# Kernel tuning notes

Hardware: AMD Instinct MI355X
Metric: run time of the kernel (lower is better)

Reference implementation:

```python
import jax, jax.numpy as jnp
import numpy as np

EPS = 1e-5
SLOPE = 0.01  # LeakyReLU default negative_slope
D_STATE = 16


def leaky(x):
    return jnp.where(x >= 0, x, SLOPE * x)


def instance_norm(x):
    # InstanceNorm3d(affine=False): normalize per (n, c) over spatial dims
    m = x.mean(axis=(2, 3, 4), keepdims=True)
    v = x.var(axis=(2, 3, 4), keepdims=True)
    return (x - m) * jax.lax.rsqrt(v + EPS)


def conv3d(x, w, b, groups=1, pad=0):
    y = jax.lax.conv_general_dilated(
        x, w, (1, 1, 1), [(pad, pad)] * 3,
        dimension_numbers=('NCDHW', 'OIDHW', 'NCDHW'),
        feature_group_count=groups)
    return y + b[None, :, None, None, None]


def conv_transpose2(x, w, b):
    # ConvTranspose3d(k=2, s=2): non-overlapping, so it is a pure einsum+interleave
    # x: [n,c,d,h,w], w: [c,o,2,2,2] (torch layout)
    y = jnp.einsum('ncdhw,coijk->nodihjwk', x, w)
    n, o, d, _, h, _, ww, _ = y.shape
    return y.reshape(n, o, 2 * d, 2 * h, 2 * ww) + b[None, :, None, None, None]


def selective_scan(u, dt, A, B, C, D):
    # u, dt: [b,l,d]; A: [d,n]; B, C: [b,l,n]; D: [d]
    dA = jnp.exp(dt[..., None] * A)                              # [b,l,d,n]
    dBu = dt[..., None] * B[:, :, None, :] * u[..., None]        # [b,l,d,n]

    def step(h, inp):
        dA_t, dBu_t, C_t = inp
        h = dA_t * h + dBu_t                                     # [b,d,n]
        y = jnp.einsum('bdn,bn->bd', h, C_t)
        return h, y

    h0 = jnp.zeros((u.shape[0],) + A.shape, u.dtype)
    _, ys = jax.lax.scan(
        step, h0,
        (dA.transpose(1, 0, 2, 3), dBu.transpose(1, 0, 2, 3), C.transpose(1, 0, 2)))
    return ys.transpose(1, 0, 2) + u * D                         # [b,l,d]


def mamba_block(x, in_proj_w, conv1d_w, conv1d_b, x_proj_w,
                dt_proj_w, dt_proj_b, A_log, D_param, out_proj_w):
    # x: [b,l,c]
    dt_rank = dt_proj_w.shape[1]
    xz = x @ in_proj_w.T                                         # [b,l,2*d_inner]
    xi, z = jnp.split(xz, 2, axis=-1)
    # causal depthwise conv1d over sequence (torch pads d_conv-1 both sides, keeps [:L])
    xi_c = xi.transpose(0, 2, 1)                                 # [b,d_inner,l]
    xi_c = jax.lax.conv_general_dilated(
        xi_c, conv1d_w, (1,), [(conv1d_w.shape[-1] - 1, 0)],
        dimension_numbers=('NCH', 'OIH', 'NCH'),
        feature_group_count=xi_c.shape[1])
    xi = jax.nn.silu(xi_c + conv1d_b[None, :, None]).transpose(0, 2, 1)  # [b,l,d_inner]
    x_dbl = xi @ x_proj_w.T
    dt, B, C = jnp.split(x_dbl, [dt_rank, dt_rank + D_STATE], axis=-1)
    dt = jax.nn.softplus(dt @ dt_proj_w.T + dt_proj_b)
    A = -jnp.exp(A_log)
    y = selective_scan(xi, dt, A, B, C, D_param)
    y = y * jax.nn.silu(z)
    return y @ out_proj_w.T


def layer_norm(x, w, b):
    m = x.mean(-1, keepdims=True)
    v = x.var(-1, keepdims=True)
    return (x - m) * jax.lax.rsqrt(v + EPS) * w + b


def up_forward(x1, x2, up_w, up_b, dc1_w, dc1_b, dc2_w, dc2_b, dc3_w, dc3_b,
               ln_w, ln_b, in_proj_w, conv1d_w, conv1d_b, x_proj_w,
               dt_proj_w, dt_proj_b, A_log, D_param, out_proj_w):
    x1 = conv_transpose2(x1, up_w, up_b)
    dZ = x2.shape[2] - x1.shape[2]
    dY = x2.shape[3] - x1.shape[3]
    dX = x2.shape[4] - x1.shape[4]
    x1 = jnp.pad(x1, ((0, 0), (0, 0),
                      (dZ // 2, dZ - dZ // 2),
                      (dY // 2, dY - dY // 2),
                      (dX // 2, dX - dX // 2)))
    x = jnp.concatenate([x2, x1], axis=1)
    # DoubleConv (residual=False since in_channels != out_channels)
    x = leaky(instance_norm(conv3d(x, dc1_w, dc1_b)))
    x = leaky(instance_norm(conv3d(x, dc2_w, dc2_b, groups=8, pad=1)))
    x = leaky(instance_norm(conv3d(x, dc3_w, dc3_b)))
    # MambaLayer over flattened spatial tokens
    b, c, d, h, w = x.shape
    t = x.transpose(0, 2, 3, 4, 1).reshape(b, d * h * w, c)
    t = layer_norm(t, ln_w, ln_b)
    t = mamba_block(t, in_proj_w, conv1d_w, conv1d_b, x_proj_w,
                    dt_proj_w, dt_proj_b, A_log, D_param, out_proj_w)
    return t.reshape(b, d, h, w, c).transpose(0, 4, 1, 2, 3)


def setup_inputs() -> dict:
    key = jax.random.key(0)
    ks = jax.random.split(key, 20)
    c_out = 32      # out_channels / d_model
    d_inner = 64    # expand * d_model
    dt_rank = 2     # ceil(32/16)
    s = 0.02
    return {
        'x1': jax.random.normal(ks[0], (2, 32, 8, 16, 16), jnp.float32),
        'x2': jax.random.normal(ks[1], (2, 32, 16, 32, 32), jnp.float32),
        'up_w': jax.random.normal(ks[2], (32, 32, 2, 2, 2), jnp.float32) * s,
        'up_b': jnp.zeros((32,), jnp.float32),
        'dc1_w': jax.random.normal(ks[3], (32, 64, 1, 1, 1), jnp.float32) * s,
        'dc1_b': jnp.zeros((32,), jnp.float32),
        'dc2_w': jax.random.normal(ks[4], (32, 4, 3, 3, 3), jnp.float32) * s,
        'dc2_b': jnp.zeros((32,), jnp.float32),
        'dc3_w': jax.random.normal(ks[5], (32, 32, 1, 1, 1), jnp.float32) * s,
        'dc3_b': jnp.zeros((32,), jnp.float32),
        'ln_w': jnp.ones((c_out,), jnp.float32),
        'ln_b': jnp.zeros((c_out,), jnp.float32),
        'in_proj_w': jax.random.normal(ks[6], (2 * d_inner, c_out), jnp.float32) * s,
        'conv1d_w': jax.random.normal(ks[7], (d_inner, 1, 4), jnp.float32) * s,
        'conv1d_b': jnp.zeros((d_inner,), jnp.float32),
        'x_proj_w': jax.random.normal(ks[8], (dt_rank + 2 * D_STATE, d_inner), jnp.float32) * s,
        'dt_proj_w': jax.random.normal(ks[9], (d_inner, dt_rank), jnp.float32) * s,
        'dt_proj_b': jnp.full((d_inner,), -4.0, jnp.float32),
        'A_log': jnp.log(jnp.tile(jnp.arange(1.0, D_STATE + 1.0, dtype=jnp.float32), (d_inner, 1))),
        'D_param': jnp.ones((d_inner,), jnp.float32),
        'out_proj_w': jax.random.normal(ks[10], (c_out, d_inner), jnp.float32) * s,
    }


def reference(x1, x2, up_w, up_b, dc1_w, dc1_b, dc2_w, dc2_b, dc3_w, dc3_b,
              ln_w, ln_b, in_proj_w, conv1d_w, conv1d_b, x_proj_w,
              dt_proj_w, dt_proj_b, A_log, D_param, out_proj_w):
    return up_forward(x1, x2, up_w, up_b, dc1_w, dc1_b, dc2_w, dc2_b, dc3_w, dc3_b,
                      ln_w, ln_b, in_proj_w, conv1d_w, conv1d_b, x_proj_w,
                      dt_proj_w, dt_proj_b, A_log, D_param, out_proj_w)
```

## Files before the change

### kernel.cpp

```cpp
#include <hip/hip_runtime.h>

#define TPB 256
#define BATCH 2
#define S_TOT 16384
#define NST 16
#define NCHUNK 256
#define CLEN 64
#define EPS 1e-5f
#define SLOPE 0.01f

__device__ __forceinline__ float leakyf(float v){ return v > 0.f ? v : SLOPE * v; }
__device__ __forceinline__ float siluf(float v){ return v / (1.f + __expf(-v)); }

__global__ __launch_bounds__(TPB) void k_up(
    const float* __restrict__ x1, const float* __restrict__ upw,
    const float* __restrict__ upb, float* __restrict__ up) {
  __shared__ float wq[2048];
  int t = threadIdx.x;
  int idx = blockIdx.x * TPB + t;
  int s = idx & 16383;
  int n = (idx >> 14) & 1;
  int q = idx >> 15;
  for (int i = t; i < 2048; i += TPB) {
    int c = i >> 6;
    wq[i] = upw[c*256 + q*64 + (i & 63)];
  }
  __syncthreads();
  int z = s >> 10, y = (s >> 5) & 31, x = s & 31;
  int tap = ((z & 1)*2 + (y & 1))*2 + (x & 1);
  int xb = n*65536 + (z >> 1)*256 + (y >> 1)*16 + (x >> 1);
  float xv[32];
  #pragma unroll
  for (int c = 0; c < 32; c++) xv[c] = x1[xb + c*2048];
  float acc[8];
  #pragma unroll
  for (int j = 0; j < 8; j++) acc[j] = upb[q*8 + j];
  #pragma unroll
  for (int c = 0; c < 32; c++) {
    #pragma unroll
    for (int j = 0; j < 8; j++)
      acc[j] += xv[c] * wq[c*64 + j*8 + tap];
  }
  #pragma unroll
  for (int j = 0; j < 8; j++)
    up[(n*32 + q*8 + j)*S_TOT + s] = acc[j];
}

__global__ __launch_bounds__(TPB) void k_conv1(
    const float* __restrict__ x2, const float* __restrict__ up,
    const float* __restrict__ w, const float* __restrict__ bias,
    float* __restrict__ c1, float* __restrict__ st1) {
  __shared__ float ws[512];
  __shared__ float red[4][8][2];
  int t = threadIdx.x;
  int idx = blockIdx.x * TPB + t;
  int s = idx & 16383;
  int n = (idx >> 14) & 1;
  int q = idx >> 15;
  int c0 = q*8;
  for (int i = t; i < 512; i += TPB) ws[i] = w[c0*64 + i];
  __syncthreads();
  const float* px2 = x2 + n*32*S_TOT + s;
  const float* pup = up + n*32*S_TOT + s;
  float acc[8];
  #pragma unroll
  for (int j = 0; j < 8; j++) acc[j] = bias[c0 + j];
  #pragma unroll
  for (int i = 0; i < 32; i++) {
    float v = px2[i*S_TOT];
    #pragma unroll
    for (int j = 0; j < 8; j++) acc[j] += v * ws[j*64 + i];
  }
  #pragma unroll
  for (int i = 0; i < 32; i++) {
    float v = pup[i*S_TOT];
    #pragma unroll
    for (int j = 0; j < 8; j++) acc[j] += v * ws[j*64 + 32 + i];
  }
  #pragma unroll
  for (int j = 0; j < 8; j++)
    c1[(n*32 + c0 + j)*S_TOT + s] = acc[j];
  int wv = t >> 6;
  #pragma unroll
  for (int j = 0; j < 8; j++) {
    float sm = acc[j], sq = acc[j]*acc[j];
    #pragma unroll
    for (int o = 32; o > 0; o >>= 1) { sm += __shfl_down(sm, o); sq += __shfl_down(sq, o); }
    if ((t & 63) == 0) { red[wv][j][0] = sm; red[wv][j][1] = sq; }
  }
  __syncthreads();
  if (t < 16) {
    int j = t >> 1, m = t & 1;
    float a = red[0][j][m] + red[1][j][m] + red[2][j][m] + red[3][j][m];
    atomicAdd(&st1[(n*32 + c0 + j)*2 + m], a);
  }
}

__global__ __launch_bounds__(TPB) void k_pad(
    const float* __restrict__ c1, const float* __restrict__ st1,
    float* __restrict__ pn) {
  int slice = blockIdx.y;
  int i = blockIdx.x * TPB + threadIdx.x;
  if (i >= 20808) return;
  float s0 = st1[slice*2], s1 = st1[slice*2 + 1];
  float m = s0 * (1.f/S_TOT);
  float rs = rsqrtf(s1*(1.f/S_TOT) - m*m + EPS);
  int zp = i / 1156; int r = i - zp*1156; int yp = r / 34; int xp = r - yp*34;
  float v = 0.f;
  if (zp >= 1 && zp <= 16 && yp >= 1 && yp <= 32 && xp >= 1 && xp <= 32)
    v = leakyf((c1[slice*S_TOT + (zp-1)*1024 + (yp-1)*32 + (xp-1)] - m) * rs);
  pn[slice*20808 + i] = v;
}

__global__ __launch_bounds__(TPB) void k_conv2(
    const float* __restrict__ pn, const float* __restrict__ w,
    const float* __restrict__ bias, float* __restrict__ c2,
    float* __restrict__ st2) {
  __shared__ float ws[432];
  __shared__ float red[4][4][2];
  int bid = blockIdx.x, t = threadIdx.x;
  int s = ((bid & 63) << 8) + t;
  int g = (bid >> 6) & 7;
  int n = bid >> 9;
  for (int i = t; i < 432; i += TPB) ws[i] = w[(g*4)*108 + i];
  __syncthreads();
  int z = s >> 10, y = (s >> 5) & 31, x = s & 31;
  float acc[4];
  #pragma unroll
  for (int oc = 0; oc < 4; oc++) acc[oc] = bias[g*4 + oc];
  const float* pbase = pn + ((n*32 + g*4)*18)*1156;
  #pragma unroll
  for (int ic = 0; ic < 4; ic++) {
    const float* pc = pbase + ic*(18*1156);
    #pragma unroll
    for (int dz = 0; dz < 3; dz++) {
      #pragma unroll
      for (int dy = 0; dy < 3; dy++) {
        const float* pr = pc + (z+dz)*1156 + (y+dy)*34 + x;
        float p0 = pr[0], p1 = pr[1], p2 = pr[2];
        int wb = ic*27 + dz*9 + dy*3;
        #pragma unroll
        for (int oc = 0; oc < 4; oc++) {
          const float* wo = &ws[oc*108 + wb];
          acc[oc] += p0*wo[0] + p1*wo[1] + p2*wo[2];
        }
      }
    }
  }
  float sm[4], sq[4];
  #pragma unroll
  for (int oc = 0; oc < 4; oc++) {
    c2[(n*32 + g*4 + oc)*S_TOT + s] = acc[oc];
    sm[oc] = acc[oc]; sq[oc] = acc[oc]*acc[oc];
  }
  #pragma unroll
  for (int o = 32; o > 0; o >>= 1) {
    #pragma unroll
    for (int oc = 0; oc < 4; oc++) {
      sm[oc] += __shfl_down(sm[oc], o);
      sq[oc] += __shfl_down(sq[oc], o);
    }
  }
  int lane = t & 63, wv = t >> 6;
  if (lane == 0) {
    #pragma unroll
    for (int oc = 0; oc < 4; oc++) { red[wv][oc][0] = sm[oc]; red[wv][oc][1] = sq[oc]; }
  }
  __syncthreads();
  if (t < 8) {
    int oc = t & 3, m = t >> 2;
    float a = red[0][oc][m] + red[1][oc][m] + red[2][oc][m] + red[3][oc][m];
    atomicAdd(&st2[(n*32 + g*4 + oc)*2 + m], a);
  }
}

__global__ __launch_bounds__(TPB) void k_conv3(
    const float* __restrict__ c2, const float* __restrict__ w,
    const float* __restrict__ bias, const float* __restrict__ st2,
    float* __restrict__ c3, float* __restrict__ st3) {
  __shared__ float ws[256];
  __shared__ float mrs[32][2];
  __shared__ float red[4][8][2];
  int t = threadIdx.x;
  int idx = blockIdx.x * TPB + t;
  int s = idx & 16383;
  int n = (idx >> 14) & 1;
  int q = idx >> 15;
  int c0 = q*8;
  if (t < 256) ws[t] = w[c0*32 + t];
  if (t < 32) {
    float s0 = st2[(n*32+t)*2], s1 = st2[(n*32+t)*2+1];
    float m = s0 * (1.f/S_TOT);
    mrs[t][0] = m; mrs[t][1] = rsqrtf(s1*(1.f/S_TOT) - m*m + EPS);
  }
  __syncthreads();
  const float* pin = c2 + n*32*S_TOT + s;
  float acc[8];
  #pragma unroll
  for (int j = 0; j < 8; j++) acc[j] = bias[c0 + j];
  #pragma unroll
  for (int i = 0; i < 32; i++) {
    float v = leakyf((pin[i*S_TOT] - mrs[i][0]) * mrs[i][1]);
    #pragma unroll
    for (int j = 0; j < 8; j++) acc[j] += v * ws[j*32 + i];
  }
  #pragma unroll
  for (int j = 0; j < 8; j++)
    c3[(n*32 + c0 + j)*S_TOT + s] = acc[j];
  int wv = t >> 6;
  #pragma unroll
  for (int j = 0; j < 8; j++) {
    float sm = acc[j], sq = acc[j]*acc[j];
    #pragma unroll
    for (int o = 32; o > 0; o >>= 1) { sm += __shfl_down(sm, o); sq += __shfl_down(sq, o); }
    if ((t & 63) == 0) { red[wv][j][0] = sm; red[wv][j][1] = sq; }
  }
  __syncthreads();
  if (t < 16) {
    int j = t >> 1, m = t & 1;
    float a = red[0][j][m] + red[1][j][m] + red[2][j][m] + red[3][j][m];
    atomicAdd(&st3[(n*32 + c0 + j)*2 + m], a);
  }
}

__global__ __launch_bounds__(TPB) void k_inproj(
    const float* __restrict__ c3, const float* __restrict__ st3,
    const float* __restrict__ lnw, const float* __restrict__ lnb,
    const float* __restrict__ ipw,
    float* __restrict__ xi, float* __restrict__ zb) {
  __shared__ float W2T[4096];
  __shared__ float tk[16*33];
  __shared__ float S1[128], S2[128];
  __shared__ float mv[16][2];
  __shared__ float mrs[32][2];
  int t = threadIdx.x;
  int token0 = blockIdx.x * 16;
  int n = token0 >> 14;
  int s0 = token0 & 16383;
  if (t < 32) {
    float a = st3[(n*32+t)*2], b = st3[(n*32+t)*2+1];
    float m = a * (1.f/S_TOT);
    mrs[t][0] = m; mrs[t][1] = rsqrtf(b*(1.f/S_TOT) - m*m + EPS);
  }
  __syncthreads();
  for (int i = t; i < 4096; i += TPB) {
    int f = i >> 5, c = i & 31;
    W2T[c*128 + f] = ipw[i] * lnw[c];
  }
  for (int i = t; i < 512; i += TPB) {
    int c = i >> 4, lt = i & 15;
    float raw = c3[(n*32 + c)*S_TOT + s0 + lt];
    tk[lt*33 + c] = leakyf((raw - mrs[c][0]) * mrs[c][1]);
  }
  __syncthreads();
  if (t < 128) {
    float a = 0.f, b = 0.f;
    #pragma unroll
    for (int c = 0; c < 32; c++) { a += W2T[c*128 + t]; b += ipw[t*32 + c]*lnb[c]; }
    S1[t] = a; S2[t] = b;
  }
  if (t < 16) {
    float mean = 0.f;
    #pragma unroll
    for (int c = 0; c < 32; c++) mean += tk[t*33 + c];
    mean *= (1.f/32.f);
    float var = 0.f;
    #pragma unroll
    for (int c = 0; c < 32; c++) { float d = tk[t*33 + c] - mean; var += d*d; }
    mv[t][0] = mean; mv[t][1] = rsqrtf(var*(1.f/32.f) + EPS);
  }
  __syncthreads();
  int f = t & 127, half = t >> 7;
  for (int lt = half; lt < 16; lt += 2) {
    float acc = 0.f;
    #pragma unroll
    for (int c = 0; c < 32; c++) acc += W2T[c*128 + f] * tk[lt*33 + c];
    float r = mv[lt][1]*(acc - mv[lt][0]*S1[f]) + S2[f];
    int token = token0 + lt;
    if (f < 64) xi[token*64 + f] = r;
    else        zb[token*64 + (f - 64)] = r;
  }
}

__global__ __launch_bounds__(TPB) void k_conv1d(
    const float* __restrict__ xi, const float* __restrict__ c1w,
    const float* __restrict__ c1b, const float* __restrict__ xpw,
    const float* __restrict__ dtw, const float* __restrict__ dtbi,
    float* __restrict__ u, float* __restrict__ dt,
    float* __restrict__ Bb, float* __restrict__ Cc) {
  __shared__ float xpT[2176];
  __shared__ float uu[16*64];
  __shared__ float xd[16*34];
  int t = threadIdx.x;
  int token0 = blockIdx.x * 16;
  for (int i = t; i < 2176; i += TPB) { int f = i >> 6, dd = i & 63; xpT[dd*34 + f] = xpw[i]; }
  int ch = t & 63;
  float cw0 = c1w[ch*4], cw1 = c1w[ch*4+1], cw2 = c1w[ch*4+2], cw3 = c1w[ch*4+3];
  float cb = c1b[ch];
  #pragma unroll
  for (int r = 0; r < 4; r++) {
    int lt = (t >> 6) + 4*r;
    int token = token0 + lt;
    int n = token >> 14, s = token & 16383;
    int base = (n << 14)*64;
    float acc = cb;
    float v0 = (s >= 3) ? xi[base + (s-3)*64 + ch] : 0.f;
    float v1 = (s >= 2) ? xi[base + (s-2)*64 + ch] : 0.f;
    float v2 = (s >= 1) ? xi[base + (s-1)*64 + ch] : 0.f;
    float v3 = xi[base + s*64 + ch];
    acc += v0*cw0 + v1*cw1 + v2*cw2 + v3*cw3;
    float uv = siluf(acc);
    u[token*64 + ch] = uv;
    uu[lt*64 + ch] = uv;
  }
  __syncthreads();
  for (int i = t; i < 544; i += TPB) {
    int lt = i / 34; int f = i - lt*34;
    float a = 0.f;
    #pragma unroll
    for (int dd = 0; dd < 64; dd++) a += xpT[dd*34 + f] * uu[lt*64 + dd];
    xd[lt*34 + f] = a;
  }
  __syncthreads();
  float dw0 = dtw[ch*2], dw1 = dtw[ch*2+1], dbv = dtbi[ch];
  #pragma unroll
  for (int r = 0; r < 4; r++) {
    int lt = (t >> 6) + 4*r;
    int token = token0 + lt;
    float dv = xd[lt*34]*dw0 + xd[lt*34+1]*dw1 + dbv;
    dt[token*64 + ch] = fmaxf(dv, 0.f) + log1pf(__expf(-fabsf(dv)));
    if (ch < 16)      Bb[token*16 + ch]      = xd[lt*34 + 2 + ch];
    else if (ch < 32) Cc[token*16 + ch - 16] = xd[lt*34 + 2 + ch];
  }
}


__global__ __launch_bounds__(TPB) void k_scan1(
    const float* __restrict__ dt, const float* __restrict__ u,
    const float* __restrict__ Bb, const float* __restrict__ Alog,
    float* __restrict__ cA, float* __restrict__ cX) {
  __shared__ __align__(16) float sdt[1024], su[1024], sB[256];
  int bid = blockIdx.x, t = threadIdx.x;
  int chunk = bid & 255, b = bid >> 8;
  int q = t & 3, d = t >> 2;
  float Ar[4];
  #pragma unroll
  for (int j = 0; j < 4; j++) Ar[j] = -__expf(Alog[d*16 + 4*q + j]);
  float h[4] = {0.f,0.f,0.f,0.f};
  float sdts = 0.f;
  int tg0 = b*S_TOT + chunk*CLEN;
  for (int tile = 0; tile < 4; tile++) {
    int base = tg0 + tile*16;
    for (int i = t; i < 1024; i += TPB) { sdt[i] = dt[base*64 + i]; su[i] = u[base*64 + i]; }
    sB[t] = Bb[base*16 + t];
    __syncthreads();
    #pragma unroll
    for (int tt = 0; tt < 16; tt++) {
      float dtv = sdt[tt*64 + d], uv = su[tt*64 + d];
      sdts += dtv;
      float du = dtv * uv;
      float4 Bq = *(const float4*)(sB + tt*16 + q*4);
      h[0] = __expf(Ar[0]*dtv)*h[0] + Bq.x*du;
      h[1] = __expf(Ar[1]*dtv)*h[1] + Bq.y*du;
      h[2] = __expf(Ar[2]*dtv)*h[2] + Bq.z*du;
      h[3] = __expf(Ar[3]*dtv)*h[3] + Bq.w*du;
    }
    __syncthreads();
  }
  #pragma unroll
  for (int j = 0; j < 4; j++) {
    int idx = (((b*64 + d)*16 + 4*q + j)*NCHUNK) + chunk;
    cA[idx] = __expf(Ar[j]*sdts);
    cX[idx] = h[j];
  }
}

__global__ __launch_bounds__(TPB) void k_scan2(
    const float* __restrict__ cA, float* __restrict__ cX) {
  int t = threadIdx.x;
  int w = blockIdx.x*4 + (t >> 6);
  int lane = t & 63;
  int b = w >> 10, d = (w >> 4) & 63, nn = w & 15;
  int base = ((b*64 + d)*16 + nn)*NCHUNK;
  float4 a = *(const float4*)(cA + base + lane*4);
  float4 x = *(const float4*)(cX + base + lane*4);
  float A = a.x*a.y*a.z*a.w;
  float X = ((x.x*a.y + x.y)*a.z + x.z)*a.w + x.w;
  #pragma unroll
  for (int off = 1; off < 64; off <<= 1) {
    float Ap = __shfl_up(A, off);
    float Xp = __shfl_up(X, off);
    if (lane >= off) { X = A*Xp + X; A = A*Ap; }
  }
  float Xe = __shfl_up(X, 1);
  if (lane == 0) Xe = 0.f;
  float r = Xe;
  float4 o;
  o.x = r; r = a.x*r + x.x;
  o.y = r; r = a.y*r + x.y;
  o.z = r; r = a.z*r + x.z;
  o.w = r;
  *(float4*)(cX + base + lane*4) = o;
}

__global__ __launch_bounds__(TPB) void k_scan3(
    const float* __restrict__ dt, const float* __restrict__ u,
    const float* __restrict__ Bb, const float* __restrict__ Cc,
    const float* __restrict__ Alog, const float* __restrict__ Dp,
    const float* __restrict__ zb, const float* __restrict__ cX,
    float* __restrict__ g) {
  __shared__ __align__(16) float sdt[1024], su[1024], sz[1024], sB[256], sC[256];
  int bid = blockIdx.x, t = threadIdx.x;
  int chunk = bid & 255, b = bid >> 8;
  int q = t & 3, d = t >> 2;
  float Ar[4];
  #pragma unroll
  for (int j = 0; j < 4; j++) Ar[j] = -__expf(Alog[d*16 + 4*q + j]);
  float h[4];
  #pragma unroll
  for (int j = 0; j < 4; j++)
    h[j] = cX[(((b*64 + d)*16 + 4*q + j)*NCHUNK) + chunk];
  float Dv = Dp[d];
  int tg0 = b*S_TOT + chunk*CLEN;
  float* grow = g + (b*64 + d)*S_TOT + chunk*CLEN;
  for (int tile = 0; tile < 4; tile++) {
    int base = tg0 + tile*16;
    for (int i = t; i < 1024; i += TPB) {
      sdt[i] = dt[base*64 + i]; su[i] = u[base*64 + i]; sz[i] = zb[base*64 + i];
    }
    sB[t] = Bb[base*16 + t];
    sC[t] = Cc[base*16 + t];
    __syncthreads();
    #pragma unroll
    for (int tt = 0; tt < 16; tt++) {
      float dtv = sdt[tt*64 + d], uv = su[tt*64 + d];
      float du = dtv * uv;
      float4 Bq = *(const float4*)(sB + tt*16 + q*4);
      float4 Cq = *(const float4*)(sC + tt*16 + q*4);
      h[0] = __expf(Ar[0]*dtv)*h[0] + Bq.x*du;
      h[1] = __expf(Ar[1]*dtv)*h[1] + Bq.y*du;
      h[2] = __expf(Ar[2]*dtv)*h[2] + Bq.z*du;
      h[3] = __expf(Ar[3]*dtv)*h[3] + Bq.w*du;
      float yp = h[0]*Cq.x + h[1]*Cq.y + h[2]*Cq.z + h[3]*Cq.w;
      yp += __shfl_xor(yp, 1);
      yp += __shfl_xor(yp, 2);
      if (q == 0) {
        float zv = sz[tt*64 + d];
        grow[tile*16 + tt] = (yp + uv*Dv) * siluf(zv);
      }
    }
    __syncthreads();
  }
}

__global__ __launch_bounds__(TPB) void k_out(
    const float* __restrict__ g, const float* __restrict__ opw,
    float* __restrict__ out) {
  __shared__ float ws[512];
  int t = threadIdx.x;
  int idx = blockIdx.x * TPB + t;
  int s = idx & 16383;
  int n = (idx >> 14) & 1;
  int q = idx >> 15;
  int c0 = q*8;
  for (int i = t; i < 512; i += TPB) ws[i] = opw[c0*64 + i];
  __syncthreads();
  const float* pg = g + n*64*S_TOT + s;
  float acc[8] = {0.f,0.f,0.f,0.f,0.f,0.f,0.f,0.f};
  #pragma unroll
  for (int dd = 0; dd < 64; dd++) {
    float v = pg[dd*S_TOT];
    #pragma unroll
    for (int j = 0; j < 8; j++) acc[j] += v * ws[j*64 + dd];
  }
  #pragma unroll
  for (int j = 0; j < 8; j++)
    out[(n*32 + c0 + j)*S_TOT + s] = acc[j];
}

extern "C" void kernel_launch(void* const* d_in, const int* in_sizes, int n_in,
                              void* d_out, int out_size, void* d_ws, size_t ws_size,
                              hipStream_t stream) {
  const float* x1    = (const float*)d_in[0];
  const float* x2    = (const float*)d_in[1];
  const float* upw   = (const float*)d_in[2];
  const float* upb   = (const float*)d_in[3];
  const float* dc1w  = (const float*)d_in[4];
  const float* dc1b  = (const float*)d_in[5];
  const float* dc2w  = (const float*)d_in[6];
  const float* dc2b  = (const float*)d_in[7];
  const float* dc3w  = (const float*)d_in[8];
  const float* dc3b  = (const float*)d_in[9];
  const float* lnw   = (const float*)d_in[10];
  const float* lnb   = (const float*)d_in[11];
  const float* ipw   = (const float*)d_in[12];
  const float* c1w   = (const float*)d_in[13];
  const float* c1b   = (const float*)d_in[14];
  const float* xpw   = (const float*)d_in[15];
  const float* dtw   = (const float*)d_in[16];
  const float* dtbi  = (const float*)d_in[17];
  const float* Alog  = (const float*)d_in[18];
  const float* Dp    = (const float*)d_in[19];
  const float* opw   = (const float*)d_in[20];
  float* out = (float*)d_out;

  float* ws = (float*)d_ws;
  float* ubuf = ws + 0;
  float* c1   = ws + 1048576;
  float* pn   = ws + 2097152;
  float* c2   = ws + 3428864;
  float* c3   = ws + 0;
  float* xi   = ws + 1048576;
  float* zb   = ws + 4477440;
  float* ub   = ws + 6574592;
  float* dtb  = ws + 8671744;
  float* Bb   = ws + 3428864;
  float* Cc   = ws + 3953152;
  float* cA   = ws + 0;
  float* cX   = ws + 524288;
  float* gbuf = ws + 1048576;
  float* st   = ws + 10768896;
  float* st1 = st, *st2 = st + 128, *st3 = st + 256;

  hipMemsetAsync(st, 0, 384*sizeof(float), stream);
  k_up     <<<512,  TPB, 0, stream>>>(x1, upw, upb, ubuf);
  k_conv1  <<<512,  TPB, 0, stream>>>(x2, ubuf, dc1w, dc1b, c1, st1);
  k_pad    <<<dim3(82,64), TPB, 0, stream>>>(c1, st1, pn);
  k_conv2  <<<1024, TPB, 0, stream>>>(pn, dc2w, dc2b, c2, st2);
  k_conv3  <<<512,  TPB, 0, stream>>>(c2, dc3w, dc3b, st2, c3, st3);
  k_inproj <<<2048, TPB, 0, stream>>>(c3, st3, lnw, lnb, ipw, xi, zb);
  k_conv1d <<<2048, TPB, 0, stream>>>(xi, c1w, c1b, xpw, dtw, dtbi, ub, dtb, Bb, Cc);
  k_scan1  <<<512,  TPB, 0, stream>>>(dtb, ub, Bb, Alog, cA, cX);
  k_scan2  <<<512,  TPB, 0, stream>>>(cA, cX);
  k_scan3  <<<512,  TPB, 0, stream>>>(dtb, ub, Bb, Cc, Alog, Dp, zb, cX, gbuf);
  k_out    <<<512,  TPB, 0, stream>>>(gbuf, opw, out);
}
```

Baseline: 247.0 us.

## Fuse pipeline into five kernels with grid-synced single-pass scan

Fuses the transposed-conv upsample into conv1, removes the padded-normalize pass by applying InstanceNorm and zero padding inside conv2, and merges in_proj with conv1d/x_proj/dt using a 3-token halo. The three scan kernels and the output projection become one persistent kernel that uses spin-wait barriers on global atomic counters for the cross-chunk carry scan. Instance-norm statistics move from atomics to per-block partial buffers reduced by the consumer kernel. This cuts launches and intermediate global traffic. The spin barriers depend on all 512 blocks being co-resident, and the counters are reset in the previous kernel.

New measurement: 372.5 us. 1.51x slower.

```diff
diff --git a/kernel.cpp b/kernel.cpp
--- a/kernel.cpp
+++ b/kernel.cpp
@@ -1,30 +1,27 @@
 #include <hip/hip_runtime.h>
 
 #define TPB 256
-#define BATCH 2
 #define S_TOT 16384
-#define NST 16
-#define NCHUNK 256
-#define CLEN 64
 #define EPS 1e-5f
 #define SLOPE 0.01f
 
 __device__ __forceinline__ float leakyf(float v){ return v > 0.f ? v : SLOPE * v; }
 __device__ __forceinline__ float siluf(float v){ return v / (1.f + __expf(-v)); }
 
-__global__ __launch_bounds__(TPB) void k_up(
-    const float* __restrict__ x1, const float* __restrict__ upw,
-    const float* __restrict__ upb, float* __restrict__ up) {
-  __shared__ float wq[2048];
-  int t = threadIdx.x;
-  int idx = blockIdx.x * TPB + t;
-  int s = idx & 16383;
-  int n = (idx >> 14) & 1;
-  int q = idx >> 15;
-  for (int i = t; i < 2048; i += TPB) {
-    int c = i >> 6;
-    wq[i] = upw[c*256 + q*64 + (i & 63)];
-  }
+__global__ __launch_bounds__(TPB) void k_upc1(
+    const float* __restrict__ x1, const float* __restrict__ x2,
+    const float* __restrict__ upw, const float* __restrict__ upb,
+    const float* __restrict__ w1, const float* __restrict__ b1,
+    float* __restrict__ c1, float* st1p) {
+  __shared__ float wq[8192];
+  __shared__ float ws[512];
+  __shared__ float sup[64*33];
+  __shared__ float red[4][8][2];
+  int t = threadIdx.x, bid = blockIdx.x;
+  int sb = bid & 255, n = bid >> 8;
+  int p = t & 63, os = t >> 6;
+  int s = sb*64 + p;
+  for (int i = t; i < 8192; i += TPB) wq[i] = upw[i];
   __syncthreads();
   int z = s >> 10, y = (s >> 5) & 31, x = s & 31;
   int tap = ((z & 1)*2 + (y & 1))*2 + (x & 1);
@@ -32,50 +29,35 @@
   float xv[32];
   #pragma unroll
   for (int c = 0; c < 32; c++) xv[c] = x1[xb + c*2048];
+  float up[8];
+  #pragma unroll
+  for (int j = 0; j < 8; j++) up[j] = upb[os*8 + j];
+  #pragma unroll
+  for (int c = 0; c < 32; c++) {
+    #pragma unroll
+    for (int j = 0; j < 8; j++)
+      up[j] += xv[c] * wq[c*256 + (os*8 + j)*8 + tap];
+  }
+  #pragma unroll
+  for (int j = 0; j < 8; j++) sup[p*33 + os*8 + j] = up[j];
+  for (int i = t; i < 512; i += TPB) ws[i] = 0.f;
+  __syncthreads();
+  int c0 = os*8;
   float acc[8];
   #pragma unroll
-  for (int j = 0; j < 8; j++) acc[j] = upb[q*8 + j];
-  #pragma unroll
-  for (int c = 0; c < 32; c++) {
-    #pragma unroll
-    for (int j = 0; j < 8; j++)
-      acc[j] += xv[c] * wq[c*64 + j*8 + tap];
-  }
-  #pragma unroll
-  for (int j = 0; j < 8; j++)
-    up[(n*32 + q*8 + j)*S_TOT + s] = acc[j];
-}
-
-__global__ __launch_bounds__(TPB) void k_conv1(
-    const float* __restrict__ x2, const float* __restrict__ up,
-    const float* __restrict__ w, const float* __restrict__ bias,
-    float* __restrict__ c1, float* __restrict__ st1) {
-  __shared__ float ws[512];
-  __shared__ float red[4][8][2];
-  int t = threadIdx.x;
-  int idx = blockIdx.x * TPB + t;
-  int s = idx & 16383;
-  int n = (idx >> 14) & 1;
-  int q = idx >> 15;
-  int c0 = q*8;
-  for (int i = t; i < 512; i += TPB) ws[i] = w[c0*64 + i];
-  __syncthreads();
+  for (int j = 0; j < 8; j++) acc[j] = b1[c0 + j];
   const float* px2 = x2 + n*32*S_TOT + s;
-  const float* pup = up + n*32*S_TOT + s;
-  float acc[8];
-  #pragma unroll
-  for (int j = 0; j < 8; j++) acc[j] = bias[c0 + j];
   #pragma unroll
   for (int i = 0; i < 32; i++) {
     float v = px2[i*S_TOT];
     #pragma unroll
-    for (int j = 0; j < 8; j++) acc[j] += v * ws[j*64 + i];
-  }
-  #pragma unroll
-  for (int i = 0; i < 32; i++) {
-    float v = pup[i*S_TOT];
-    #pragma unroll
-    for (int j = 0; j < 8; j++) acc[j] += v * ws[j*64 + 32 + i];
+    for (int j = 0; j < 8; j++) acc[j] += v * w1[(c0 + j)*64 + i];
+  }
+  #pragma unroll
+  for (int o = 0; o < 32; o++) {
+    float v = sup[p*33 + o];
+    #pragma unroll
+    for (int j = 0; j < 8; j++) acc[j] += v * w1[(c0 + j)*64 + 32 + o];
   }
   #pragma unroll
   for (int j = 0; j < 8; j++)
@@ -89,55 +71,67 @@
     if ((t & 63) == 0) { red[wv][j][0] = sm; red[wv][j][1] = sq; }
   }
   __syncthreads();
-  if (t < 16) {
-    int j = t >> 1, m = t & 1;
-    float a = red[0][j][m] + red[1][j][m] + red[2][j][m] + red[3][j][m];
-    atomicAdd(&st1[(n*32 + c0 + j)*2 + m], a);
+  if (t < 64) {
+    int w2 = t >> 4, j = (t >> 1) & 7, m = t & 1;
+    st1p[((n*32 + w2*8 + j)*2 + m)*256 + sb] = red[w2][j][m];
   }
 }
 
-__global__ __launch_bounds__(TPB) void k_pad(
-    const float* __restrict__ c1, const float* __restrict__ st1,
-    float* __restrict__ pn) {
-  int slice = blockIdx.y;
-  int i = blockIdx.x * TPB + threadIdx.x;
-  if (i >= 20808) return;
-  float s0 = st1[slice*2], s1 = st1[slice*2 + 1];
-  float m = s0 * (1.f/S_TOT);
-  float rs = rsqrtf(s1*(1.f/S_TOT) - m*m + EPS);
-  int zp = i / 1156; int r = i - zp*1156; int yp = r / 34; int xp = r - yp*34;
-  float v = 0.f;
-  if (zp >= 1 && zp <= 16 && yp >= 1 && yp <= 32 && xp >= 1 && xp <= 32)
-    v = leakyf((c1[slice*S_TOT + (zp-1)*1024 + (yp-1)*32 + (xp-1)] - m) * rs);
-  pn[slice*20808 + i] = v;
-}
-
 __global__ __launch_bounds__(TPB) void k_conv2(
-    const float* __restrict__ pn, const float* __restrict__ w,
-    const float* __restrict__ bias, float* __restrict__ c2,
-    float* __restrict__ st2) {
+    const float* __restrict__ c1, const float* __restrict__ w,
+    const float* __restrict__ bias, const float* st1p,
+    float* __restrict__ c2, float* st2p) {
   __shared__ float ws[432];
+  __shared__ float smom[4][2];
+  __shared__ float mrs[4][2];
   __shared__ float red[4][4][2];
   int bid = blockIdx.x, t = threadIdx.x;
-  int s = ((bid & 63) << 8) + t;
-  int g = (bid >> 6) & 7;
-  int n = bid >> 9;
+  int sb = bid & 63, g = (bid >> 6) & 7, n = bid >> 9;
+  int s = (sb << 8) + t;
   for (int i = t; i < 432; i += TPB) ws[i] = w[(g*4)*108 + i];
+  {
+    int pp = t >> 5, l = t & 31;
+    if (pp < 8) {
+      int j = pp & 3, m = pp >> 2;
+      const float* sp = st1p + ((n*32 + g*4 + j)*2 + m)*256;
+      float v = 0.f;
+      #pragma unroll
+      for (int k = 0; k < 8; k++) v += sp[l + 32*k];
+      v += __shfl_down(v, 16); v += __shfl_down(v, 8); v += __shfl_down(v, 4);
+      v += __shfl_down(v, 2);  v += __shfl_down(v, 1);
+      if (l == 0) smom[j][m] = v;
+    }
+  }
+  __syncthreads();
+  if (t < 4) {
+    float m = smom[t][0] * (1.f/S_TOT);
+    mrs[t][0] = m; mrs[t][1] = rsqrtf(smom[t][1]*(1.f/S_TOT) - m*m + EPS);
+  }
   __syncthreads();
   int z = s >> 10, y = (s >> 5) & 31, x = s & 31;
+  float mx0 = (x > 0) ? 1.f : 0.f, mx2 = (x < 31) ? 1.f : 0.f;
   float acc[4];
   #pragma unroll
   for (int oc = 0; oc < 4; oc++) acc[oc] = bias[g*4 + oc];
-  const float* pbase = pn + ((n*32 + g*4)*18)*1156;
+  const float* pbase = c1 + (n*32 + g*4)*S_TOT;
   #pragma unroll
   for (int ic = 0; ic < 4; ic++) {
-    const float* pc = pbase + ic*(18*1156);
+    const float* pc = pbase + ic*S_TOT;
+    float m = mrs[ic][0], rs = mrs[ic][1];
     #pragma unroll
     for (int dz = 0; dz < 3; dz++) {
+      int zz = z + dz - 1;
+      int zc = zz < 0 ? 0 : (zz > 15 ? 15 : zz);
+      float vz = (zz >= 0 && zz < 16) ? 1.f : 0.f;
       #pragma unroll
       for (int dy = 0; dy < 3; dy++) {
-        const float* pr = pc + (z+dz)*1156 + (y+dy)*34 + x;
-        float p0 = pr[0], p1 = pr[1], p2 = pr[2];
+        int yy = y + dy - 1;
+        int yc = yy < 0 ? 0 : (yy > 31 ? 31 : yy);
+        float vzy = vz * ((yy >= 0 && yy < 32) ? 1.f : 0.f);
+        const float* pr = pc + zc*1024 + yc*32 + x;
+        float p0 = leakyf((pr[-1] - m)*rs) * (vzy*mx0);
+        float p1 = leakyf((pr[ 0] - m)*rs) * vzy;
+        float p2 = leakyf((pr[ 1] - m)*rs) * (vzy*mx2);
         int wb = ic*27 + dz*9 + dy*3;
         #pragma unroll
         for (int oc = 0; oc < 4; oc++) {
@@ -170,15 +164,16 @@
   if (t < 8) {
     int oc = t & 3, m = t >> 2;
     float a = red[0][oc][m] + red[1][oc][m] + red[2][oc][m] + red[3][oc][m];
-    atomicAdd(&st2[(n*32 + g*4 + oc)*2 + m], a);
+    st2p[((n*32 + g*4 + oc)*2 + m)*64 + sb] = a;
   }
 }
 
 __global__ __launch_bounds__(TPB) void k_conv3(
     const float* __restrict__ c2, const float* __restrict__ w,
-    const float* __restrict__ bias, const float* __restrict__ st2,
-    float* __restrict__ c3, float* __restrict__ st3) {
+    const float* __restrict__ bias, const float* st2p,
+    float* __restrict__ c3, float* st3p) {
   __shared__ float ws[256];
+  __shared__ float ssum[32][2];
   __shared__ float mrs[32][2];
   __shared__ float red[4][8][2];
   int t = threadIdx.x;
@@ -186,12 +181,21 @@
   int s = idx & 16383;
   int n = (idx >> 14) & 1;
   int q = idx >> 15;
+  int sb = blockIdx.x & 63;
   int c0 = q*8;
   if (t < 256) ws[t] = w[c0*32 + t];
+  if (t < 64) {
+    int c = t >> 1, m = t & 1;
+    const float* sp = st2p + ((n*32 + c)*2 + m)*64;
+    float v = 0.f;
+    #pragma unroll
+    for (int k = 0; k < 64; k++) v += sp[k];
+    ssum[c][m] = v;
+  }
+  __syncthreads();
   if (t < 32) {
-    float s0 = st2[(n*32+t)*2], s1 = st2[(n*32+t)*2+1];
-    float m = s0 * (1.f/S_TOT);
-    mrs[t][0] = m; mrs[t][1] = rsqrtf(s1*(1.f/S_TOT) - m*m + EPS);
+    float m = ssum[t][0] * (1.f/S_TOT);
+    mrs[t][0] = m; mrs[t][1] = rsqrtf(ssum[t][1]*(1.f/S_TOT) - m*m + EPS);
   }
   __syncthreads();
   const float* pin = c2 + n*32*S_TOT + s;
@@ -219,263 +223,248 @@
   if (t < 16) {
     int j = t >> 1, m = t & 1;
     float a = red[0][j][m] + red[1][j][m] + red[2][j][m] + red[3][j][m];
-    atomicAdd(&st3[(n*32 + c0 + j)*2 + m], a);
+    st3p[((n*32 + c0 + j)*2 + m)*64 + sb] = a;
   }
 }
 
-__global__ __launch_bounds__(TPB) void k_inproj(
-    const float* __restrict__ c3, const float* __restrict__ st3,
+__global__ __launch_bounds__(TPB) void k_token(
+    const float* __restrict__ c3, const float* st3p,
     const float* __restrict__ lnw, const float* __restrict__ lnb,
-    const float* __restrict__ ipw,
-    float* __restrict__ xi, float* __restrict__ zb) {
+    const float* __restrict__ ipw, const float* __restrict__ c1w,
+    const float* __restrict__ c1b, const float* __restrict__ xpw,
+    const float* __restrict__ dtw, const float* __restrict__ dtbi,
+    float* __restrict__ zb, float* __restrict__ u, float* __restrict__ dt,
+    float* __restrict__ Bb, float* __restrict__ Cc, int* ctrs) {
   __shared__ float W2T[4096];
-  __shared__ float tk[16*33];
+  __shared__ float xpT[2176];
+  __shared__ float tk[19*33];
+  __shared__ float sxi[19*64];
+  __shared__ float su2[16*65];
+  __shared__ float xd[16*34];
   __shared__ float S1[128], S2[128];
-  __shared__ float mv[16][2];
+  __shared__ float mv[19][2];
   __shared__ float mrs[32][2];
-  int t = threadIdx.x;
-  int token0 = blockIdx.x * 16;
-  int n = token0 >> 14;
-  int s0 = token0 & 16383;
-  if (t < 32) {
-    float a = st3[(n*32+t)*2], b = st3[(n*32+t)*2+1];
-    float m = a * (1.f/S_TOT);
-    mrs[t][0] = m; mrs[t][1] = rsqrtf(b*(1.f/S_TOT) - m*m + EPS);
-  }
-  __syncthreads();
+  __shared__ float ssum[32][2];
+  int t = threadIdx.x, bid = blockIdx.x;
+  if (bid == 0 && t < 16) ctrs[t] = 0;
+  int tok0 = bid * 16;
+  int n = tok0 >> 14, s0 = tok0 & 16383;
+  if (t < 64) {
+    int c = t >> 1, m = t & 1;
+    const float* sp = st3p + ((n*32 + c)*2 + m)*64;
+    float v = 0.f;
+    #pragma unroll
+    for (int k = 0; k < 64; k++) v += sp[k];
+    ssum[c][m] = v;
+  }
   for (int i = t; i < 4096; i += TPB) {
     int f = i >> 5, c = i & 31;
     W2T[c*128 + f] = ipw[i] * lnw[c];
   }
-  for (int i = t; i < 512; i += TPB) {
-    int c = i >> 4, lt = i & 15;
-    float raw = c3[(n*32 + c)*S_TOT + s0 + lt];
+  for (int i = t; i < 2176; i += TPB) {
+    int f = i >> 6, dd = i & 63;
+    xpT[dd*34 + f] = xpw[i];
+  }
+  __syncthreads();
+  if (t < 32) {
+    float m = ssum[t][0] * (1.f/S_TOT);
+    mrs[t][0] = m; mrs[t][1] = rsqrtf(ssum[t][1]*(1.f/S_TOT) - m*m + EPS);
+  }
+  if (t < 128) {
+    float a = 0.f, b2 = 0.f;
+    #pragma unroll
+    for (int c = 0; c < 32; c++) { a += W2T[c*128 + t]; b2 += ipw[t*32 + c]*lnb[c]; }
+    S1[t] = a; S2[t] = b2;
+  }
+  __syncthreads();
+  for (int i = t; i < 608; i += TPB) {
+    int lt = i >> 5, c = i & 31;
+    int sg = s0 - 3 + lt;
+    int sgc = sg < 0 ? 0 : sg;
+    float raw = c3[(n*32 + c)*S_TOT + sgc];
     tk[lt*33 + c] = leakyf((raw - mrs[c][0]) * mrs[c][1]);
   }
   __syncthreads();
-  if (t < 128) {
-    float a = 0.f, b = 0.f;
-    #pragma unroll
-    for (int c = 0; c < 32; c++) { a += W2T[c*128 + t]; b += ipw[t*32 + c]*lnb[c]; }
-    S1[t] = a; S2[t] = b;
-  }
-  if (t < 16) {
+  if (t < 19) {
     float mean = 0.f;
     #pragma unroll
     for (int c = 0; c < 32; c++) mean += tk[t*33 + c];
     mean *= (1.f/32.f);
     float var = 0.f;
     #pragma unroll
-    for (int c = 0; c < 32; c++) { float d = tk[t*33 + c] - mean; var += d*d; }
+    for (int c = 0; c < 32; c++) { float d2 = tk[t*33 + c] - mean; var += d2*d2; }
     mv[t][0] = mean; mv[t][1] = rsqrtf(var*(1.f/32.f) + EPS);
   }
   __syncthreads();
-  int f = t & 127, half = t >> 7;
-  for (int lt = half; lt < 16; lt += 2) {
+  for (int i = t; i < 19*128; i += TPB) {
+    int lt = i >> 7, f = i & 127;
     float acc = 0.f;
     #pragma unroll
     for (int c = 0; c < 32; c++) acc += W2T[c*128 + f] * tk[lt*33 + c];
     float r = mv[lt][1]*(acc - mv[lt][0]*S1[f]) + S2[f];
-    int token = token0 + lt;
-    if (f < 64) xi[token*64 + f] = r;
-    else        zb[token*64 + (f - 64)] = r;
-  }
-}
-
-__global__ __launch_bounds__(TPB) void k_conv1d(
-    const float* __restrict__ xi, const float* __restrict__ c1w,
-    const float* __restrict__ c1b, const float* __restrict__ xpw,
-    const float* __restrict__ dtw, const float* __restrict__ dtbi,
-    float* __restrict__ u, float* __restrict__ dt,
-    float* __restrict__ Bb, float* __restrict__ Cc) {
-  __shared__ float xpT[2176];
-  __shared__ float uu[16*64];
-  __shared__ float xd[16*34];
-  int t = threadIdx.x;
-  int token0 = blockIdx.x * 16;
-  for (int i = t; i < 2176; i += TPB) { int f = i >> 6, dd = i & 63; xpT[dd*34 + f] = xpw[i]; }
+    int sg = s0 - 3 + lt;
+    if (f < 64) {
+      sxi[lt*64 + f] = (sg < 0) ? 0.f : r;
+    } else if (lt >= 3) {
+      zb[(tok0 + lt - 3)*64 + (f - 64)] = r;
+    }
+  }
+  __syncthreads();
   int ch = t & 63;
   float cw0 = c1w[ch*4], cw1 = c1w[ch*4+1], cw2 = c1w[ch*4+2], cw3 = c1w[ch*4+3];
   float cb = c1b[ch];
   #pragma unroll
   for (int r = 0; r < 4; r++) {
     int lt = (t >> 6) + 4*r;
-    int token = token0 + lt;
-    int n = token >> 14, s = token & 16383;
-    int base = (n << 14)*64;
-    float acc = cb;
-    float v0 = (s >= 3) ? xi[base + (s-3)*64 + ch] : 0.f;
-    float v1 = (s >= 2) ? xi[base + (s-2)*64 + ch] : 0.f;
-    float v2 = (s >= 1) ? xi[base + (s-1)*64 + ch] : 0.f;
-    float v3 = xi[base + s*64 + ch];
-    acc += v0*cw0 + v1*cw1 + v2*cw2 + v3*cw3;
+    float acc = cb + sxi[lt*64 + ch]*cw0 + sxi[(lt+1)*64 + ch]*cw1
+                   + sxi[(lt+2)*64 + ch]*cw2 + sxi[(lt+3)*64 + ch]*cw3;
     float uv = siluf(acc);
-    u[token*64 + ch] = uv;
-    uu[lt*64 + ch] = uv;
+    u[(tok0 + lt)*64 + ch] = uv;
+    su2[lt*65 + ch] = uv;
   }
   __syncthreads();
   for (int i = t; i < 544; i += TPB) {
-    int lt = i / 34; int f = i - lt*34;
+    int lt = i / 34, f = i - lt*34;
     float a = 0.f;
     #pragma unroll
-    for (int dd = 0; dd < 64; dd++) a += xpT[dd*34 + f] * uu[lt*64 + dd];
+    for (int dd = 0; dd < 64; dd++) a += xpT[dd*34 + f] * su2[lt*65 + dd];
     xd[lt*34 + f] = a;
   }
   __syncthreads();
-  float dw0 = dtw[ch*2], dw1 = dtw[ch*2+1], dbv = dtbi[ch];
+  float dw0 = dtw[ch*2], dw1 = dtw[ch*2+1], db = dtbi[ch];
   #pragma unroll
   for (int r = 0; r < 4; r++) {
     int lt = (t >> 6) + 4*r;
-    int token = token0 + lt;
-    float dv = xd[lt*34]*dw0 + xd[lt*34+1]*dw1 + dbv;
+    int token = tok0 + lt;
+    float dv = xd[lt*34]*dw0 + xd[lt*34 + 1]*dw1 + db;
     dt[token*64 + ch] = fmaxf(dv, 0.f) + log1pf(__expf(-fabsf(dv)));
     if (ch < 16)      Bb[token*16 + ch]      = xd[lt*34 + 2 + ch];
     else if (ch < 32) Cc[token*16 + ch - 16] = xd[lt*34 + 2 + ch];
   }
 }
 
-
-__global__ __launch_bounds__(TPB) void k_scan1(
-    const float* __restrict__ dt, const float* __restrict__ u,
-    const float* __restrict__ Bb, const float* __restrict__ Alog,
-    float* __restrict__ cA, float* __restrict__ cX) {
-  __shared__ __align__(16) float sdt[1024], su[1024], sB[256];
-  int bid = blockIdx.x, t = threadIdx.x;
-  int chunk = bid & 255, b = bid >> 8;
-  int q = t & 3, d = t >> 2;
-  float Ar[4];
-  #pragma unroll
-  for (int j = 0; j < 4; j++) Ar[j] = -__expf(Alog[d*16 + 4*q + j]);
-  float h[4] = {0.f,0.f,0.f,0.f};
-  float sdts = 0.f;
-  int tg0 = b*S_TOT + chunk*CLEN;
-  for (int tile = 0; tile < 4; tile++) {
-    int base = tg0 + tile*16;
-    for (int i = t; i < 1024; i += TPB) { sdt[i] = dt[base*64 + i]; su[i] = u[base*64 + i]; }
-    sB[t] = Bb[base*16 + t];
-    __syncthreads();
-    #pragma unroll
-    for (int tt = 0; tt < 16; tt++) {
-      float dtv = sdt[tt*64 + d], uv = su[tt*64 + d];
-      sdts += dtv;
-      float du = dtv * uv;
-      float4 Bq = *(const float4*)(sB + tt*16 + q*4);
-      h[0] = __expf(Ar[0]*dtv)*h[0] + Bq.x*du;
-      h[1] = __expf(Ar[1]*dtv)*h[1] + Bq.y*du;
-      h[2] = __expf(Ar[2]*dtv)*h[2] + Bq.z*du;
-      h[3] = __expf(Ar[3]*dtv)*h[3] + Bq.w*du;
-    }
-    __syncthreads();
-  }
-  #pragma unroll
-  for (int j = 0; j < 4; j++) {
-    int idx = (((b*64 + d)*16 + 4*q + j)*NCHUNK) + chunk;
-    cA[idx] = __expf(Ar[j]*sdts);
-    cX[idx] = h[j];
-  }
-}
-
-__global__ __launch_bounds__(TPB) void k_scan2(
-    const float* __restrict__ cA, float* __restrict__ cX) {
-  int t = threadIdx.x;
-  int w = blockIdx.x*4 + (t >> 6);
-  int lane = t & 63;
-  int b = w >> 10, d = (w >> 4) & 63, nn = w & 15;
-  int base = ((b*64 + d)*16 + nn)*NCHUNK;
-  float4 a = *(const float4*)(cA + base + lane*4);
-  float4 x = *(const float4*)(cX + base + lane*4);
-  float A = a.x*a.y*a.z*a.w;
-  float X = ((x.x*a.y + x.y)*a.z + x.z)*a.w + x.w;
-  #pragma unroll
-  for (int off = 1; off < 64; off <<= 1) {
-    float Ap = __shfl_up(A, off);
-    float Xp = __shfl_up(X, off);
-    if (lane >= off) { X = A*Xp + X; A = A*Ap; }
-  }
-  float Xe = __shfl_up(X, 1);
-  if (lane == 0) Xe = 0.f;
-  float r = Xe;
-  float4 o;
-  o.x = r; r = a.x*r + x.x;
-  o.y = r; r = a.y*r + x.y;
-  o.z = r; r = a.z*r + x.z;
-  o.w = r;
-  *(float4*)(cX + base + lane*4) = o;
-}
-
-__global__ __launch_bounds__(TPB) void k_scan3(
+__global__ __launch_bounds__(TPB, 2) void k_scan(
     const float* __restrict__ dt, const float* __restrict__ u,
     const float* __restrict__ Bb, const float* __restrict__ Cc,
     const float* __restrict__ Alog, const float* __restrict__ Dp,
-    const float* __restrict__ zb, const float* __restrict__ cX,
-    float* __restrict__ g) {
-  __shared__ __align__(16) float sdt[1024], su[1024], sz[1024], sB[256], sC[256];
-  int bid = blockIdx.x, t = threadIdx.x;
+    const float* __restrict__ zb, const float* __restrict__ opw,
+    float* aggA, float* aggX, float* seedX, int* ctrs,
+    float* __restrict__ out) {
+  __shared__ float sdt[4096], su[4096], sB[1024], sC[1024];
+  __shared__ float gt[64*65];
+  int t = threadIdx.x, bid = blockIdx.x;
   int chunk = bid & 255, b = bid >> 8;
   int q = t & 3, d = t >> 2;
+  int tok0 = b*S_TOT + chunk*64;
+  for (int i = t; i < 4096; i += TPB) {
+    sdt[i] = dt[tok0*64 + i];
+    su[i]  = u[tok0*64 + i];
+    gt[(i >> 6)*65 + (i & 63)] = zb[tok0*64 + i];
+  }
+  for (int i = t; i < 1024; i += TPB) { sB[i] = Bb[tok0*16 + i]; sC[i] = Cc[tok0*16 + i]; }
   float Ar[4];
   #pragma unroll
   for (int j = 0; j < 4; j++) Ar[j] = -__expf(Alog[d*16 + 4*q + j]);
-  float h[4];
-  #pragma unroll
-  for (int j = 0; j < 4; j++)
-    h[j] = cX[(((b*64 + d)*16 + 4*q + j)*NCHUNK) + chunk];
   float Dv = Dp[d];
-  int tg0 = b*S_TOT + chunk*CLEN;
-  float* grow = g + (b*64 + d)*S_TOT + chunk*CLEN;
-  for (int tile = 0; tile < 4; tile++) {
-    int base = tg0 + tile*16;
-    for (int i = t; i < 1024; i += TPB) {
-      sdt[i] = dt[base*64 + i]; su[i] = u[base*64 + i]; sz[i] = zb[base*64 + i];
-    }
-    sB[t] = Bb[base*16 + t];
-    sC[t] = Cc[base*16 + t];
-    __syncthreads();
-    #pragma unroll
-    for (int tt = 0; tt < 16; tt++) {
-      float dtv = sdt[tt*64 + d], uv = su[tt*64 + d];
-      float du = dtv * uv;
-      float4 Bq = *(const float4*)(sB + tt*16 + q*4);
-      float4 Cq = *(const float4*)(sC + tt*16 + q*4);
-      h[0] = __expf(Ar[0]*dtv)*h[0] + Bq.x*du;
-      h[1] = __expf(Ar[1]*dtv)*h[1] + Bq.y*du;
-      h[2] = __expf(Ar[2]*dtv)*h[2] + Bq.z*du;
-      h[3] = __expf(Ar[3]*dtv)*h[3] + Bq.w*du;
-      float yp = h[0]*Cq.x + h[1]*Cq.y + h[2]*Cq.z + h[3]*Cq.w;
-      yp += __shfl_xor(yp, 1);
-      yp += __shfl_xor(yp, 2);
-      if (q == 0) {
-        float zv = sz[tt*64 + d];
-        grow[tile*16 + tt] = (yp + uv*Dv) * siluf(zv);
-      }
-    }
-    __syncthreads();
-  }
-}
-
-__global__ __launch_bounds__(TPB) void k_out(
-    const float* __restrict__ g, const float* __restrict__ opw,
-    float* __restrict__ out) {
-  __shared__ float ws[512];
-  int t = threadIdx.x;
-  int idx = blockIdx.x * TPB + t;
-  int s = idx & 16383;
-  int n = (idx >> 14) & 1;
-  int q = idx >> 15;
-  int c0 = q*8;
-  for (int i = t; i < 512; i += TPB) ws[i] = opw[c0*64 + i];
-  __syncthreads();
-  const float* pg = g + n*64*S_TOT + s;
-  float acc[8] = {0.f,0.f,0.f,0.f,0.f,0.f,0.f,0.f};
-  #pragma unroll
-  for (int dd = 0; dd < 64; dd++) {
-    float v = pg[dd*S_TOT];
-    #pragma unroll
-    for (int j = 0; j < 8; j++) acc[j] += v * ws[j*64 + dd];
-  }
-  #pragma unroll
-  for (int j = 0; j < 8; j++)
-    out[(n*32 + c0 + j)*S_TOT + s] = acc[j];
+  __syncthreads();
+  float h0 = 0.f, h1 = 0.f, h2 = 0.f, h3 = 0.f, sd = 0.f;
+  for (int tt = 0; tt < 64; tt++) {
+    float dtv = sdt[tt*64 + d], uv = su[tt*64 + d];
+    sd += dtv;
+    float du = dtv * uv;
+    float4 Bq = *(const float4*)(sB + tt*16 + q*4);
+    h0 = __expf(Ar[0]*dtv)*h0 + Bq.x*du;
+    h1 = __expf(Ar[1]*dtv)*h1 + Bq.y*du;
+    h2 = __expf(Ar[2]*dtv)*h2 + Bq.z*du;
+    h3 = __expf(Ar[3]*dtv)*h3 + Bq.w*du;
+  }
+  {
+    float4 av; av.x = __expf(Ar[0]*sd); av.y = __expf(Ar[1]*sd);
+    av.z = __expf(Ar[2]*sd); av.w = __expf(Ar[3]*sd);
+    float4 xv4; xv4.x = h0; xv4.y = h1; xv4.z = h2; xv4.w = h3;
+    *(float4*)(aggA + (size_t)bid*1024 + t*4) = av;
+    *(float4*)(aggX + (size_t)bid*1024 + t*4) = xv4;
+  }
+  __syncthreads();
+  if (t == 0) {
+    __threadfence();
+    atomicAdd(&ctrs[0], 1);
+    while (__hip_atomic_load(&ctrs[0], __ATOMIC_ACQUIRE, __HIP_MEMORY_SCOPE_AGENT) < 512)
+      __builtin_amdgcn_s_sleep(2);
+  }
+  __syncthreads();
+  {
+    int wv = t >> 6, lane = t & 63;
+    int seq = bid*4 + wv;
+    int qb = seq >> 10, eoff = seq & 1023;
+    float a4[4], x4[4];
+    #pragma unroll
+    for (int k = 0; k < 4; k++) {
+      int slot = qb*256 + lane*4 + k;
+      a4[k] = aggA[(size_t)slot*1024 + eoff];
+      x4[k] = aggX[(size_t)slot*1024 + eoff];
+    }
+    float A = a4[0]*a4[1]*a4[2]*a4[3];
+    float X = ((x4[0]*a4[1] + x4[1])*a4[2] + x4[2])*a4[3] + x4[3];
+    #pragma unroll
+    for (int off = 1; off < 64; off <<= 1) {
+      float Ap = __shfl_up(A, off), Xp = __shfl_up(X, off);
+      if (lane >= off) { X = A*Xp + X; A = A*Ap; }
+    }
+    float Xe = __shfl_up(X, 1);
+    if (lane == 0) Xe = 0.f;
+    float r = Xe;
+    #pragma unroll
+    for (int k = 0; k < 4; k++) {
+      int slot = qb*256 + lane*4 + k;
+      seedX[(size_t)slot*1024 + eoff] = r;
+      r = a4[k]*r + x4[k];
+    }
+  }
+  __syncthreads();
+  if (t == 0) {
+    __threadfence();
+    atomicAdd(&ctrs[1], 1);
+    while (__hip_atomic_load(&ctrs[1], __ATOMIC_ACQUIRE, __HIP_MEMORY_SCOPE_AGENT) < 512)
+      __builtin_amdgcn_s_sleep(2);
+  }
+  __syncthreads();
+  {
+    float4 hs = *(const float4*)(seedX + (size_t)bid*1024 + t*4);
+    h0 = hs.x; h1 = hs.y; h2 = hs.z; h3 = hs.w;
+  }
+  for (int tt = 0; tt < 64; tt++) {
+    float dtv = sdt[tt*64 + d], uv = su[tt*64 + d];
+    float du = dtv * uv;
+    float4 Bq = *(const float4*)(sB + tt*16 + q*4);
+    float4 Cq = *(const float4*)(sC + tt*16 + q*4);
+    h0 = __expf(Ar[0]*dtv)*h0 + Bq.x*du;
+    h1 = __expf(Ar[1]*dtv)*h1 + Bq.y*du;
+    h2 = __expf(Ar[2]*dtv)*h2 + Bq.z*du;
+    h3 = __expf(Ar[3]*dtv)*h3 + Bq.w*du;
+    float yp = h0*Cq.x + h1*Cq.y + h2*Cq.z + h3*Cq.w;
+    yp += __shfl_xor(yp, 1);
+    yp += __shfl_xor(yp, 2);
+    if (q == 0) {
+      float zv = gt[tt*65 + d];
+      gt[tt*65 + d] = (yp + uv*Dv) * siluf(zv);
+    }
+  }
+  __syncthreads();
+  {
+    int sl = t & 63, cb = t >> 6;
+    float acc[8] = {0.f,0.f,0.f,0.f,0.f,0.f,0.f,0.f};
+    const float* wp = opw + cb*8*64;
+    #pragma unroll
+    for (int dd = 0; dd < 64; dd++) {
+      float v = gt[sl*65 + dd];
+      #pragma unroll
+      for (int j = 0; j < 8; j++) acc[j] += v * wp[j*64 + dd];
+    }
+    #pragma unroll
+    for (int j = 0; j < 8; j++)
+      out[(b*32 + cb*8 + j)*S_TOT + chunk*64 + sl] = acc[j];
+  }
 }
 
 extern "C" void kernel_launch(void* const* d_in, const int* in_sizes, int n_in,
@@ -505,33 +494,27 @@
   float* out = (float*)d_out;
 
   float* ws = (float*)d_ws;
-  float* ubuf = ws + 0;
-  float* c1   = ws + 1048576;
-  float* pn   = ws + 2097152;
-  float* c2   = ws + 3428864;
-  float* c3   = ws + 0;
-  float* xi   = ws + 1048576;
-  float* zb   = ws + 4477440;
-  float* ub   = ws + 6574592;
-  float* dtb  = ws + 8671744;
-  float* Bb   = ws + 3428864;
-  float* Cc   = ws + 3953152;
-  float* cA   = ws + 0;
-  float* cX   = ws + 524288;
-  float* gbuf = ws + 1048576;
-  float* st   = ws + 10768896;
-  float* st1 = st, *st2 = st + 128, *st3 = st + 256;
-
-  hipMemsetAsync(st, 0, 384*sizeof(float), stream);
-  k_up     <<<512,  TPB, 0, stream>>>(x1, upw, upb, ubuf);
-  k_conv1  <<<512,  TPB, 0, stream>>>(x2, ubuf, dc1w, dc1b, c1, st1);
-  k_pad    <<<dim3(82,64), TPB, 0, stream>>>(c1, st1, pn);
-  k_conv2  <<<1024, TPB, 0, stream>>>(pn, dc2w, dc2b, c2, st2);
-  k_conv3  <<<512,  TPB, 0, stream>>>(c2, dc3w, dc3b, st2, c3, st3);
-  k_inproj <<<2048, TPB, 0, stream>>>(c3, st3, lnw, lnb, ipw, xi, zb);
-  k_conv1d <<<2048, TPB, 0, stream>>>(xi, c1w, c1b, xpw, dtw, dtbi, ub, dtb, Bb, Cc);
-  k_scan1  <<<512,  TPB, 0, stream>>>(dtb, ub, Bb, Alog, cA, cX);
-  k_scan2  <<<512,  TPB, 0, stream>>>(cA, cX);
-  k_scan3  <<<512,  TPB, 0, stream>>>(dtb, ub, Bb, Cc, Alog, Dp, zb, cX, gbuf);
-  k_out    <<<512,  TPB, 0, stream>>>(gbuf, opw, out);
+  float* st1p  = ws + 0;
+  float* st2p  = ws + 32768;
+  float* st3p  = ws + 40960;
+  int*   ctrs  = (int*)(ws + 49152);
+  float* c1    = ws + 49168;
+  float* c2    = ws + 1097744;
+  float* c3    = ws + 2146320;
+  float* zb    = ws + 3194896;
+  float* ub    = ws + 5292048;
+  float* dtb   = ws + 7389200;
+  float* Bb    = ws + 9486352;
+  float* Cc    = ws + 10010640;
+  float* aggA  = ws + 10534928;
+  float* aggX  = ws + 11059216;
+  float* seedX = ws + 11583504;
+
+  k_upc1 <<<512,  TPB, 0, stream>>>(x1, x2, upw, upb, dc1w, dc1b, c1, st1p);
+  k_conv2<<<1024, TPB, 0, stream>>>(c1, dc2w, dc2b, st1p, c2, st2p);
+  k_conv3<<<512,  TPB, 0, stream>>>(c2, dc3w, dc3b, st2p, c3, st3p);
+  k_token<<<2048, TPB, 0, stream>>>(c3, st3p, lnw, lnb, ipw, c1w, c1b, xpw,
+                                    dtw, dtbi, zb, ub, dtb, Bb, Cc, ctrs);
+  k_scan <<<512,  TPB, 0, stream>>>(dtb, ub, Bb, Cc, Alog, Dp, zb, opw,
+                                    aggA, aggX, seedX, ctrs, out);
 }
```
